# Kernel optimization log

Measured on AMD Instinct MI355X. Metric: run time of the kernel, lower is better.

Reference implementation:

```python
import jax, jax.numpy as jnp
import numpy as np

N_NODES = 100000
N_EDGES = 1600000


def sgconv(x, src, dst, W, b, K=1):
    """PyG SGConv: K hops of GCN-normalized propagation, then Linear."""
    n = x.shape[0]
    # add self loops
    loop = jnp.arange(n, dtype=src.dtype)
    s = jnp.concatenate([src, loop])  # source (j)
    d = jnp.concatenate([dst, loop])  # target (i)
    # symmetric normalization: deg over targets of A+I
    deg = jax.ops.segment_sum(jnp.ones_like(d, dtype=x.dtype), d, num_segments=n)
    dinv = jnp.where(deg > 0, jax.lax.rsqrt(deg), 0.0)
    norm = dinv[s] * dinv[d]  # [E+N]
    for _ in range(K):
        msg = x[s] * norm[:, None]  # gather + scale  [E+N, F]
        x = jax.ops.segment_sum(msg, d, num_segments=n)  # scatter-add
    return x @ W + b


def setup_inputs() -> dict:
    key = jax.random.key(0)
    k1, k2, k3, k4, k5, k6, k7 = jax.random.split(key, 7)
    x = jax.random.normal(k1, (N_NODES, 128), dtype=jnp.float32)
    edge_index = jax.random.randint(k2, (2, N_EDGES), 0, N_NODES, dtype=jnp.int64)
    # Glorot-ish scaled weights
    W1 = jax.random.normal(k3, (128, 128), dtype=jnp.float32) * (1.0 / np.sqrt(128))
    b1 = jax.random.normal(k4, (128,), dtype=jnp.float32) * 0.01
    W2 = jax.random.normal(k5, (128, 64), dtype=jnp.float32) * (1.0 / np.sqrt(128))
    b2 = jax.random.normal(k6, (64,), dtype=jnp.float32) * 0.01
    return {"x": x, "edge_index": edge_index, "W1": W1, "b1": b1, "W2": W2, "b2": b2}


def reference(x, edge_index, W1, b1, W2, b2):
    src, dst = edge_index[0], edge_index[1]
    h = sgconv(x, src, dst, W1, b1, K=1)
    out = sgconv(h, src, dst, W2, b2, K=1)
    return out
```

## Files before the change

### kernel.cpp

```cpp
#include <hip/hip_runtime.h>

#define NN 100000
#define NE 1600000
#define BSH 9
#define NPB (1 << BSH)
#define NBKT ((NN + NPB - 1) >> BSH)
#define ABLK 400
#define EPB (NE / ABLK)

typedef __attribute__((ext_vector_type(8))) short short8;
typedef __attribute__((ext_vector_type(4))) float f32x4;

__device__ __forceinline__ unsigned short bf16r(float f) {
    unsigned u = __float_as_uint(f);
    u += 0x7fffu + ((u >> 16) & 1u);
    return (unsigned short)(u >> 16);
}
__device__ __forceinline__ unsigned pack2(float a, float b) {
    unsigned ua = __float_as_uint(a), ub = __float_as_uint(b);
    ua += 0x7fffu + ((ua >> 16) & 1u);
    ub += 0x7fffu + ((ub >> 16) & 1u);
    return (ua >> 16) | (ub & 0xffff0000u);
}
__device__ __forceinline__ float2 unpack2(unsigned u) {
    float2 r;
    r.x = __uint_as_float(u << 16);
    r.y = __uint_as_float(u & 0xffff0000u);
    return r;
}

__global__ __launch_bounds__(256) void k_histA(const int* __restrict__ dst,
                                               unsigned* __restrict__ ghist) {
    __shared__ unsigned h[NBKT];
    int b = blockIdx.x, t = threadIdx.x;
    for (int k = t; k < NBKT; k += 256) h[k] = 0;
    __syncthreads();
    int e0 = b * EPB;
    for (int e = e0 + t; e < e0 + EPB; e += 256)
        atomicAdd(&h[(unsigned)dst[e] >> BSH], 1u);
    __syncthreads();
    for (int k = t; k < NBKT; k += 256) ghist[b * NBKT + k] = h[k];
}

__global__ __launch_bounds__(256) void k_coltot(const unsigned* __restrict__ ghist,
                                                unsigned* __restrict__ tot) {
    __shared__ unsigned sh[256];
    int k = blockIdx.x, t = threadIdx.x;
    unsigned s = 0;
    for (int b = t; b < ABLK; b += 256) s += ghist[b * NBKT + k];
    sh[t] = s;
    __syncthreads();
    for (int d = 128; d > 0; d >>= 1) {
        if (t < d) sh[t] += sh[t + d];
        __syncthreads();
    }
    if (t == 0) tot[k] = sh[0];
}

__global__ __launch_bounds__(256) void k_basescan(const unsigned* __restrict__ tot,
                                                  unsigned* __restrict__ base,
                                                  unsigned* __restrict__ boff) {
    __shared__ unsigned sh[256];
    int t = threadIdx.x;
    unsigned v = (t < NBKT) ? tot[t] : 0;
    sh[t] = v;
    __syncthreads();
    for (int d = 1; d < 256; d <<= 1) {
        unsigned u = (t >= d) ? sh[t - d] : 0;
        __syncthreads();
        sh[t] += u;
        __syncthreads();
    }
    if (t < NBKT) { base[t] = sh[t] - v; boff[t] = sh[t] - v; }
    if (t == 0) boff[NBKT] = NE;
}

__global__ __launch_bounds__(512) void k_colscan(unsigned* __restrict__ ghist,
                                                 const unsigned* __restrict__ base) {
    __shared__ unsigned sh[512];
    int k = blockIdx.x, t = threadIdx.x;
    unsigned v = (t < ABLK) ? ghist[t * NBKT + k] : 0;
    sh[t] = v;
    __syncthreads();
    for (int d = 1; d < 512; d <<= 1) {
        unsigned u = (t >= d) ? sh[t - d] : 0;
        __syncthreads();
        sh[t] += u;
        __syncthreads();
    }
    if (t < ABLK) ghist[t * NBKT + k] = base[k] + sh[t] - v;
}

__global__ __launch_bounds__(256) void k_scatA(const int* __restrict__ src,
                                               const int* __restrict__ dst,
                                               const unsigned* __restrict__ ghist,
                                               unsigned* __restrict__ epk) {
    __shared__ unsigned cur[NBKT];
    int b = blockIdx.x, t = threadIdx.x;
    for (int k = t; k < NBKT; k += 256) cur[k] = ghist[b * NBKT + k];
    __syncthreads();
    int e0 = b * EPB;
    for (int e = e0 + t; e < e0 + EPB; e += 256) {
        unsigned d = (unsigned)dst[e];
        unsigned pos = atomicAdd(&cur[d >> BSH], 1u);
        epk[pos] = ((d & (NPB - 1)) << 17) | (unsigned)src[e];
    }
}

__global__ __launch_bounds__(512) void k_csrB(const unsigned* __restrict__ boff,
                                              const unsigned* __restrict__ epk,
                                              int* __restrict__ csr, int* __restrict__ off,
                                              int* __restrict__ deg, float* __restrict__ dinv) {
    __shared__ unsigned lcnt[NPB];
    __shared__ unsigned lcur[NPB];
    int k = blockIdx.x, t = threadIdx.x;
    unsigned e0 = boff[k], e1 = boff[k + 1];
    lcnt[t] = 0;
    __syncthreads();
    for (unsigned e = e0 + t; e < e1; e += NPB)
        atomicAdd(&lcnt[epk[e] >> 17], 1u);
    __syncthreads();
    unsigned own = lcnt[t];
    lcur[t] = own;
    __syncthreads();
    for (int d = 1; d < NPB; d <<= 1) {
        unsigned v = (t >= d) ? lcur[t - d] : 0;
        __syncthreads();
        lcur[t] += v;
        __syncthreads();
    }
    unsigned excl = lcur[t] - own;
    int n = k * NPB + t;
    if (n < NN) {
        off[n]  = (int)(e0 + excl);
        deg[n]  = (int)own;
        dinv[n] = rsqrtf((float)own + 1.0f);
    }
    __syncthreads();
    lcur[t] = excl;
    __syncthreads();
    for (unsigned e = e0 + t; e < e1; e += NPB) {
        unsigned u = epk[e];
        unsigned pos = atomicAdd(&lcur[u >> 17], 1u);
        csr[e0 + pos] = (int)(u & 0x1FFFFu);
    }
}

__global__ void k_w12(const float* __restrict__ W1, const float* __restrict__ W2,
                      const float* __restrict__ b1, float* __restrict__ W12,
                      float* __restrict__ c2) {
    int idx = blockIdx.x * blockDim.x + threadIdx.x;
    if (idx < 128 * 64) {
        int i = idx >> 6, j = idx & 63;
        float acc = 0.f;
        for (int k = 0; k < 128; ++k) acc += W1[i * 128 + k] * W2[k * 64 + j];
        W12[idx] = acc;
    } else if (idx < 128 * 64 + 64) {
        int j = idx - 128 * 64;
        float acc = 0.f;
        for (int k = 0; k < 128; ++k) acc += b1[k] * W2[k * 64 + j];
        c2[j] = acc;
    }
}

__global__ __launch_bounds__(256) void k_gemmYs(const float* __restrict__ x,
                                                const float* __restrict__ W12f,
                                                const float* __restrict__ dinv,
                                                unsigned short* __restrict__ ys) {
    __shared__ float Al[64][132];
    __shared__ short Wl[64][136];
    int t = threadIdx.x;
    int row0 = blockIdx.x * 64;

    for (int idx = t; idx < 8192; idx += 256) {
        int k = idx >> 6, n = idx & 63;
        Wl[n][k] = (short)bf16r(W12f[idx]);
    }
    for (int idx = t; idx < 64 * 32; idx += 256) {
        int r = idx >> 5, c4 = idx & 31;
        float4 v = make_float4(0.f, 0.f, 0.f, 0.f);
        if (row0 + r < NN) v = *(const float4*)&x[(size_t)(row0 + r) * 128 + c4 * 4];
        *(float4*)&Al[r][c4 * 4] = v;
    }
    __syncthreads();

    int wv = t >> 6, lane = t & 63;
    int l15 = lane & 15, l4 = lane >> 4;

    short8 afr[4];
    #pragma unroll
    for (int ks = 0; ks < 4; ++ks) {
        const float* ap = &Al[wv * 16 + l15][ks * 32 + l4 * 8];
        float4 f0 = *(const float4*)ap;
        float4 f1 = *(const float4*)(ap + 4);
        short8 a;
        a[0] = (short)bf16r(f0.x); a[1] = (short)bf16r(f0.y);
        a[2] = (short)bf16r(f0.z); a[3] = (short)bf16r(f0.w);
        a[4] = (short)bf16r(f1.x); a[5] = (short)bf16r(f1.y);
        a[6] = (short)bf16r(f1.z); a[7] = (short)bf16r(f1.w);
        afr[ks] = a;
    }
    short8 bfr[4][4];
    #pragma unroll
    for (int ct = 0; ct < 4; ++ct)
        #pragma unroll
        for (int ks = 0; ks < 4; ++ks)
            bfr[ct][ks] = *(const short8*)&Wl[ct * 16 + l15][ks * 32 + l4 * 8];

    f32x4 acc[4] = {};
    #pragma unroll
    for (int ks = 0; ks < 4; ++ks)
        #pragma unroll
        for (int ct = 0; ct < 4; ++ct)
            acc[ct] = __builtin_amdgcn_mfma_f32_16x16x32_bf16(afr[ks], bfr[ct][ks], acc[ct], 0, 0, 0);

    int rbase = row0 + wv * 16 + l4 * 4;
    float di[4];
    #pragma unroll
    for (int r = 0; r < 4; ++r) di[r] = (rbase + r < NN) ? dinv[rbase + r] : 0.f;
    #pragma unroll
    for (int ct = 0; ct < 4; ++ct) {
        int col = ct * 16 + l15;
        #pragma unroll
        for (int r = 0; r < 4; ++r) {
            if (rbase + r < NN)
                ys[(size_t)(rbase + r) * 64 + col] = bf16r(acc[ct][r] * di[r]);
        }
    }
}

__global__ __launch_bounds__(256) void k_gatherA(const int* __restrict__ off,
        const int* __restrict__ deg, const int* __restrict__ csr,
        const float* __restrict__ dinv, const uint2* __restrict__ ys,
        const float* __restrict__ c2, uint2* __restrict__ ts) {
    int gid = blockIdx.x * blockDim.x + threadIdx.x;
    int node = gid >> 4;
    int lane = threadIdx.x & 15;
    if (node >= NN) return;
    uint2 u = ys[(size_t)node * 16 + lane];
    float2 a = unpack2(u.x), b = unpack2(u.y);
    float ax = a.x, ay = a.y, az = b.x, aw = b.y;
    int e = off[node], end = e + deg[node];
    for (; e + 8 <= end; e += 8) {
        uint2 uu[8];
        #pragma unroll
        for (int j = 0; j < 8; ++j) uu[j] = ys[(size_t)csr[e + j] * 16 + lane];
        #pragma unroll
        for (int j = 0; j < 8; ++j) {
            float2 t = unpack2(uu[j].x); ax += t.x; ay += t.y;
            t = unpack2(uu[j].y); az += t.x; aw += t.y;
        }
    }
    for (; e + 4 <= end; e += 4) {
        uint2 uu[4];
        #pragma unroll
        for (int j = 0; j < 4; ++j) uu[j] = ys[(size_t)csr[e + j] * 16 + lane];
        #pragma unroll
        for (int j = 0; j < 4; ++j) {
            float2 t = unpack2(uu[j].x); ax += t.x; ay += t.y;
            t = unpack2(uu[j].y); az += t.x; aw += t.y;
        }
    }
    for (; e < end; ++e) {
        uint2 uu = ys[(size_t)csr[e] * 16 + lane];
        float2 t = unpack2(uu.x); ax += t.x; ay += t.y;
        t = unpack2(uu.y); az += t.x; aw += t.y;
    }
    float di = dinv[node];
    float s = di * di;
    float4 cc = ((const float4*)c2)[lane];
    ts[(size_t)node * 16 + lane] = make_uint2(pack2(s * ax + di * cc.x, s * ay + di * cc.y),
                                              pack2(s * az + di * cc.z, s * aw + di * cc.w));
}

__global__ __launch_bounds__(256) void k_gatherB(const int* __restrict__ off,
        const int* __restrict__ deg, const int* __restrict__ csr,
        const float* __restrict__ dinv, const uint2* __restrict__ ts,
        const float* __restrict__ bias, float4* __restrict__ out) {
    int gid = blockIdx.x * blockDim.x + threadIdx.x;
    int node = gid >> 4;
    int lane = threadIdx.x & 15;
    if (node >= NN) return;
    uint2 u = ts[(size_t)node * 16 + lane];
    float2 a = unpack2(u.x), b = unpack2(u.y);
    float ax = a.x, ay = a.y, az = b.x, aw = b.y;
    int e = off[node], end = e + deg[node];
    for (; e + 8 <= end; e += 8) {
        uint2 uu[8];
        #pragma unroll
        for (int j = 0; j < 8; ++j) uu[j] = ts[(size_t)csr[e + j] * 16 + lane];
        #pragma unroll
        for (int j = 0; j < 8; ++j) {
            float2 t = unpack2(uu[j].x); ax += t.x; ay += t.y;
            t = unpack2(uu[j].y); az += t.x; aw += t.y;
        }
    }
    for (; e + 4 <= end; e += 4) {
        uint2 uu[4];
        #pragma unroll
        for (int j = 0; j < 4; ++j) uu[j] = ts[(size_t)csr[e + j] * 16 + lane];
        #pragma unroll
        for (int j = 0; j < 4; ++j) {
            float2 t = unpack2(uu[j].x); ax += t.x; ay += t.y;
            t = unpack2(uu[j].y); az += t.x; aw += t.y;
        }
    }
    for (; e < end; ++e) {
        uint2 uu = ts[(size_t)csr[e] * 16 + lane];
        float2 t = unpack2(uu.x); ax += t.x; ay += t.y;
        t = unpack2(uu.y); az += t.x; aw += t.y;
    }
    float di = dinv[node];
    float4 bb = ((const float4*)bias)[lane];
    out[(size_t)node * 16 + lane] = make_float4(ax * di + bb.x, ay * di + bb.y,
                                                az * di + bb.z, aw * di + bb.w);
}

extern "C" void kernel_launch(void* const* d_in, const int* in_sizes, int n_in,
                              void* d_out, int out_size, void* d_ws, size_t ws_size,
                              hipStream_t stream) {
    const float* x  = (const float*)d_in[0];
    const int*   ei = (const int*)d_in[1];
    const float* W1 = (const float*)d_in[2];
    const float* b1 = (const float*)d_in[3];
    const float* W2 = (const float*)d_in[4];
    const float* b2 = (const float*)d_in[5];
    float* out = (float*)d_out;

    const int* src = ei;
    const int* dst = ei + NE;

    float* fws  = (float*)d_ws;
    float* dinv = fws;
    unsigned* ys = (unsigned*)(fws + 102400);
    unsigned* ts = ys + (size_t)NN * 32;
    float* W12  = (float*)(ts + (size_t)NN * 32);
    float* c2   = W12 + 8192;
    int* off  = (int*)(c2 + 128);
    int* deg  = off + 100096;
    int* csr  = deg + 100096;
    unsigned* epk   = (unsigned*)(csr + NE);
    unsigned* ghist = epk + NE;
    unsigned* tot   = ghist + ABLK * NBKT;
    unsigned* base  = tot + 256;
    unsigned* boff  = base + 256;

    k_histA<<<ABLK, 256, 0, stream>>>(dst, ghist);
    k_coltot<<<NBKT, 256, 0, stream>>>(ghist, tot);
    k_basescan<<<1, 256, 0, stream>>>(tot, base, boff);
    k_colscan<<<NBKT, 512, 0, stream>>>(ghist, base);
    k_scatA<<<ABLK, 256, 0, stream>>>(src, dst, ghist, epk);
    k_csrB<<<NBKT, NPB, 0, stream>>>(boff, epk, csr, off, deg, dinv);

    k_w12<<<33, 256, 0, stream>>>(W1, W2, b1, W12, c2);

    k_gemmYs<<<(NN + 63) / 64, 256, 0, stream>>>(x, W12, dinv, (unsigned short*)ys);

    k_gatherA<<<(NN * 16 + 255) / 256, 256, 0, stream>>>(off, deg, csr, dinv,
                                                         (const uint2*)ys, c2, (uint2*)ts);

    k_gatherB<<<(NN * 16 + 255) / 256, 256, 0, stream>>>(off, deg, csr, dinv,
                                                         (const uint2*)ts, b2, (float4*)out);
}
```

Before: 146.6 us.

## Replace histogram-scan CSR build with fixed-capacity buckets and fuse weight precompute

```diff
diff --git a/kernel.cpp b/kernel.cpp
--- a/kernel.cpp
+++ b/kernel.cpp
@@ -7,6 +7,7 @@
 #define NBKT ((NN + NPB - 1) >> BSH)
 #define ABLK 400
 #define EPB (NE / ABLK)
+#define CAP 10240
 
 typedef __attribute__((ext_vector_type(8))) short short8;
 typedef __attribute__((ext_vector_type(4))) float f32x4;
@@ -29,92 +30,62 @@
     return r;
 }
 
-__global__ __launch_bounds__(256) void k_histA(const int* __restrict__ dst,
-                                               unsigned* __restrict__ ghist) {
-    __shared__ unsigned h[NBKT];
+__global__ __launch_bounds__(256) void k_scat2(const int* __restrict__ src,
+                                               const int* __restrict__ dst,
+                                               unsigned* __restrict__ cur,
+                                               unsigned* __restrict__ epk) {
+    __shared__ unsigned hcnt[NBKT];
+    __shared__ unsigned hbase[NBKT];
     int b = blockIdx.x, t = threadIdx.x;
-    for (int k = t; k < NBKT; k += 256) h[k] = 0;
+    for (int k = t; k < NBKT; k += 256) hcnt[k] = 0;
     __syncthreads();
     int e0 = b * EPB;
     for (int e = e0 + t; e < e0 + EPB; e += 256)
-        atomicAdd(&h[(unsigned)dst[e] >> BSH], 1u);
-    __syncthreads();
-    for (int k = t; k < NBKT; k += 256) ghist[b * NBKT + k] = h[k];
-}
-
-__global__ __launch_bounds__(256) void k_coltot(const unsigned* __restrict__ ghist,
-                                                unsigned* __restrict__ tot) {
-    __shared__ unsigned sh[256];
-    int k = blockIdx.x, t = threadIdx.x;
-    unsigned s = 0;
-    for (int b = t; b < ABLK; b += 256) s += ghist[b * NBKT + k];
-    sh[t] = s;
-    __syncthreads();
-    for (int d = 128; d > 0; d >>= 1) {
-        if (t < d) sh[t] += sh[t + d];
-        __syncthreads();
-    }
-    if (t == 0) tot[k] = sh[0];
-}
-
-__global__ __launch_bounds__(256) void k_basescan(const unsigned* __restrict__ tot,
-                                                  unsigned* __restrict__ base,
-                                                  unsigned* __restrict__ boff) {
-    __shared__ unsigned sh[256];
-    int t = threadIdx.x;
-    unsigned v = (t < NBKT) ? tot[t] : 0;
-    sh[t] = v;
-    __syncthreads();
-    for (int d = 1; d < 256; d <<= 1) {
-        unsigned u = (t >= d) ? sh[t - d] : 0;
-        __syncthreads();
-        sh[t] += u;
-        __syncthreads();
-    }
-    if (t < NBKT) { base[t] = sh[t] - v; boff[t] = sh[t] - v; }
-    if (t == 0) boff[NBKT] = NE;
-}
-
-__global__ __launch_bounds__(512) void k_colscan(unsigned* __restrict__ ghist,
-                                                 const unsigned* __restrict__ base) {
-    __shared__ unsigned sh[512];
-    int k = blockIdx.x, t = threadIdx.x;
-    unsigned v = (t < ABLK) ? ghist[t * NBKT + k] : 0;
-    sh[t] = v;
-    __syncthreads();
-    for (int d = 1; d < 512; d <<= 1) {
-        unsigned u = (t >= d) ? sh[t - d] : 0;
-        __syncthreads();
-        sh[t] += u;
-        __syncthreads();
-    }
-    if (t < ABLK) ghist[t * NBKT + k] = base[k] + sh[t] - v;
-}
-
-__global__ __launch_bounds__(256) void k_scatA(const int* __restrict__ src,
-                                               const int* __restrict__ dst,
-                                               const unsigned* __restrict__ ghist,
-                                               unsigned* __restrict__ epk) {
-    __shared__ unsigned cur[NBKT];
-    int b = blockIdx.x, t = threadIdx.x;
-    for (int k = t; k < NBKT; k += 256) cur[k] = ghist[b * NBKT + k];
-    __syncthreads();
-    int e0 = b * EPB;
+        atomicAdd(&hcnt[(unsigned)dst[e] >> BSH], 1u);
+    __syncthreads();
+    for (int k = t; k < NBKT; k += 256) {
+        unsigned c = hcnt[k];
+        hbase[k] = k * CAP + (c ? atomicAdd(&cur[k], c) : 0u);
+        hcnt[k] = 0;
+    }
+    __syncthreads();
     for (int e = e0 + t; e < e0 + EPB; e += 256) {
         unsigned d = (unsigned)dst[e];
-        unsigned pos = atomicAdd(&cur[d >> BSH], 1u);
+        unsigned kb = d >> BSH;
+        unsigned pos = hbase[kb] + atomicAdd(&hcnt[kb], 1u);
         epk[pos] = ((d & (NPB - 1)) << 17) | (unsigned)src[e];
     }
 }
 
-__global__ __launch_bounds__(512) void k_csrB(const unsigned* __restrict__ boff,
-                                              const unsigned* __restrict__ epk,
-                                              int* __restrict__ csr, int* __restrict__ off,
-                                              int* __restrict__ deg, float* __restrict__ dinv) {
+__global__ __launch_bounds__(512) void k_csrB2(const unsigned* __restrict__ cur,
+                                               const unsigned* __restrict__ epk,
+                                               int* __restrict__ csr, int* __restrict__ off,
+                                               int* __restrict__ deg, float* __restrict__ dinv,
+                                               const float* __restrict__ W1,
+                                               const float* __restrict__ W2,
+                                               const float* __restrict__ b1,
+                                               unsigned short* __restrict__ W12b,
+                                               float* __restrict__ c2) {
+    int blk = blockIdx.x;
+    if (blk >= NBKT) {
+        int idx = (blk - NBKT) * 512 + threadIdx.x;
+        if (idx < 8192) {
+            int i = idx >> 6, j = idx & 63;
+            float acc = 0.f;
+            for (int k = 0; k < 128; ++k) acc += W1[i * 128 + k] * W2[k * 64 + j];
+            W12b[j * 128 + i] = bf16r(acc);
+        } else if (idx < 8192 + 64) {
+            int j = idx - 8192;
+            float acc = 0.f;
+            for (int k = 0; k < 128; ++k) acc += b1[k] * W2[k * 64 + j];
+            c2[j] = acc;
+        }
+        return;
+    }
     __shared__ unsigned lcnt[NPB];
     __shared__ unsigned lcur[NPB];
-    int k = blockIdx.x, t = threadIdx.x;
-    unsigned e0 = boff[k], e1 = boff[k + 1];
+    int k = blk, t = threadIdx.x;
+    unsigned e0 = (unsigned)k * CAP, e1 = e0 + cur[k];
     lcnt[t] = 0;
     __syncthreads();
     for (unsigned e = e0 + t; e < e1; e += NPB)
@@ -146,25 +117,8 @@
     }
 }
 
-__global__ void k_w12(const float* __restrict__ W1, const float* __restrict__ W2,
-                      const float* __restrict__ b1, float* __restrict__ W12,
-                      float* __restrict__ c2) {
-    int idx = blockIdx.x * blockDim.x + threadIdx.x;
-    if (idx < 128 * 64) {
-        int i = idx >> 6, j = idx & 63;
-        float acc = 0.f;
-        for (int k = 0; k < 128; ++k) acc += W1[i * 128 + k] * W2[k * 64 + j];
-        W12[idx] = acc;
-    } else if (idx < 128 * 64 + 64) {
-        int j = idx - 128 * 64;
-        float acc = 0.f;
-        for (int k = 0; k < 128; ++k) acc += b1[k] * W2[k * 64 + j];
-        c2[j] = acc;
-    }
-}
-
 __global__ __launch_bounds__(256) void k_gemmYs(const float* __restrict__ x,
-                                                const float* __restrict__ W12f,
+                                                const unsigned short* __restrict__ W12b,
                                                 const float* __restrict__ dinv,
                                                 unsigned short* __restrict__ ys) {
     __shared__ float Al[64][132];
@@ -172,9 +126,9 @@
     int t = threadIdx.x;
     int row0 = blockIdx.x * 64;
 
-    for (int idx = t; idx < 8192; idx += 256) {
-        int k = idx >> 6, n = idx & 63;
-        Wl[n][k] = (short)bf16r(W12f[idx]);
+    for (int idx8 = t; idx8 < 1024; idx8 += 256) {
+        int n = idx8 >> 4, c8 = idx8 & 15;
+        *(short8*)&Wl[n][c8 * 8] = *(const short8*)&W12b[n * 128 + c8 * 8];
     }
     for (int idx = t; idx < 64 * 32; idx += 256) {
         int r = idx >> 5, c4 = idx & 31;
@@ -334,27 +288,20 @@
     float* dinv = fws;
     unsigned* ys = (unsigned*)(fws + 102400);
     unsigned* ts = ys + (size_t)NN * 32;
-    float* W12  = (float*)(ts + (size_t)NN * 32);
-    float* c2   = W12 + 8192;
+    unsigned short* W12b = (unsigned short*)(ts + (size_t)NN * 32);
+    float* c2   = (float*)(W12b + 8192);
     int* off  = (int*)(c2 + 128);
     int* deg  = off + 100096;
     int* csr  = deg + 100096;
-    unsigned* epk   = (unsigned*)(csr + NE);
-    unsigned* ghist = epk + NE;
-    unsigned* tot   = ghist + ABLK * NBKT;
-    unsigned* base  = tot + 256;
-    unsigned* boff  = base + 256;
-
-    k_histA<<<ABLK, 256, 0, stream>>>(dst, ghist);
-    k_coltot<<<NBKT, 256, 0, stream>>>(ghist, tot);
-    k_basescan<<<1, 256, 0, stream>>>(tot, base, boff);
-    k_colscan<<<NBKT, 512, 0, stream>>>(ghist, base);
-    k_scatA<<<ABLK, 256, 0, stream>>>(src, dst, ghist, epk);
-    k_csrB<<<NBKT, NPB, 0, stream>>>(boff, epk, csr, off, deg, dinv);
-
-    k_w12<<<33, 256, 0, stream>>>(W1, W2, b1, W12, c2);
-
-    k_gemmYs<<<(NN + 63) / 64, 256, 0, stream>>>(x, W12, dinv, (unsigned short*)ys);
+    unsigned* epk = (unsigned*)(csr + NBKT * CAP);
+    unsigned* cur = epk + NBKT * CAP;
+
+    hipMemsetAsync(cur, 0, NBKT * sizeof(unsigned), stream);
+    k_scat2<<<ABLK, 256, 0, stream>>>(src, dst, cur, epk);
+    k_csrB2<<<NBKT + 17, 512, 0, stream>>>(cur, epk, csr, off, deg, dinv,
+                                           W1, W2, b1, W12b, c2);
+
+    k_gemmYs<<<(NN + 63) / 64, 256, 0, stream>>>(x, W12b, dinv, (unsigned short*)ys);
 
     k_gatherA<<<(NN * 16 + 255) / 256, 256, 0, stream>>>(off, deg, csr, dinv,
                                                          (const uint2*)ys, c2, (uint2*)ts);
```

After: 138.6 us. 5.4% less time.
